# Optimization experiments

Hardware: AMD Instinct MI355X
Metric: run time of the kernel (lower is better)

Reference implementation:

```python
import jax, jax.numpy as jnp
import numpy as np

N = 8192
D = 512            # d_model
E = 8              # num_experts
H = 1024           # expert_hidden_dim
RH = 256           # router_hidden_dim
TOPK = 2
IN_DIM = 9 * D + 3
LN_EPS = 1e-5


def layernorm(x, g, b, eps=LN_EPS):
    m = jnp.mean(x, axis=-1, keepdims=True)
    v = jnp.mean((x - m) ** 2, axis=-1, keepdims=True)
    return (x - m) * jax.lax.rsqrt(v + eps) * g + b


def setup_inputs() -> dict:
    key = jax.random.key(0)
    ks = jax.random.split(key, 16)
    s_in = 1.0 / np.sqrt(IN_DIM)
    s_rh = 1.0 / np.sqrt(RH)
    s_h = 1.0 / np.sqrt(H)
    return {
        "z1": jax.random.normal(ks[0], (N, D), jnp.float32),
        "z2": jax.random.normal(ks[1], (N, D), jnp.float32),
        "z3": jax.random.normal(ks[2], (N, D), jnp.float32),
        "mask": jnp.ones((N, 3), jnp.float32),
        # LayerNorms
        "ln_g": jnp.ones((D,), jnp.float32), "ln_b": jnp.zeros((D,), jnp.float32),
        "lnp_g": jnp.ones((D,), jnp.float32), "lnp_b": jnp.zeros((D,), jnp.float32),
        "oln_g": jnp.ones((D,), jnp.float32), "oln_b": jnp.zeros((D,), jnp.float32),
        # Router MLP
        "r_w1": jax.random.normal(ks[3], (IN_DIM, RH), jnp.float32) * s_in,
        "r_b1": jnp.zeros((RH,), jnp.float32),
        "r_w2": jax.random.normal(ks[4], (RH, E), jnp.float32) * s_rh,
        "r_b2": jnp.zeros((E,), jnp.float32),
        "log_temp": jnp.array(np.log(1.0), jnp.float32),
        # Stacked experts: fc1 [E, IN_DIM, H], fc2 [E, H, D]
        "e_w1": jax.random.normal(ks[5], (E, IN_DIM, H), jnp.float32) * s_in,
        "e_b1": jnp.zeros((E, H), jnp.float32),
        "e_w2": jax.random.normal(ks[6], (E, H, D), jnp.float32) * s_h,
        "e_b2": jnp.zeros((E, D), jnp.float32),
    }


def reference(z1, z2, z3, mask, ln_g, ln_b, lnp_g, lnp_b, oln_g, oln_b,
              r_w1, r_b1, r_w2, r_b2, log_temp, e_w1, e_b1, e_w2, e_b2):
    # --- build fusion input ---
    z1n = layernorm(z1, ln_g, ln_b)
    z2n = layernorm(z2, ln_g, ln_b)
    z3n = layernorm(z3, ln_g, ln_b)
    d12 = layernorm(z1n - z2n, lnp_g, lnp_b)
    d13 = layernorm(z1n - z3n, lnp_g, lnp_b)
    d23 = layernorm(z2n - z3n, lnp_g, lnp_b)
    p12 = layernorm(z1n * z2n, lnp_g, lnp_b)
    p13 = layernorm(z1n * z3n, lnp_g, lnp_b)
    p23 = layernorm(z2n * z3n, lnp_g, lnp_b)
    x = jnp.concatenate([z1n, z2n, z3n, d12, d13, d23, p12, p13, p23, mask], axis=-1)  # [N, 9D+3]

    # --- router: MLP + temperature-scaled top-k softmax ---
    temp = jnp.clip(jnp.exp(log_temp), 1e-3, 100.0)
    rh = jax.nn.gelu(x @ r_w1 + r_b1, approximate=False)
    logits = (rh @ r_w2 + r_b2) / temp                      # [N, E]
    topv, topi = jax.lax.top_k(logits, TOPK)
    keep = jnp.zeros_like(logits).at[jnp.arange(logits.shape[0])[:, None], topi].set(1.0)
    masked_logits = jnp.where(keep == 0, -jnp.inf, logits)
    gate = jax.nn.softmax(masked_logits, axis=-1)           # [N, E]

    # --- dense expert compute (matches torch.stack over experts) ---
    eh = jax.nn.gelu(jnp.einsum('ni,eih->neh', x, e_w1) + e_b1, approximate=False)
    outs = jnp.einsum('neh,ehd->ned', eh, e_w2) + e_b2      # [N, E, D]
    z = jnp.einsum('ne,ned->nd', gate, outs)                # combine

    # --- masked residual ---
    denom = jnp.clip(jnp.sum(mask, axis=1, keepdims=True), 1.0, None)
    z_res = (mask[:, 0:1] * z1n + mask[:, 1:2] * z2n + mask[:, 2:3] * z3n) / denom
    z = z + z_res

    return layernorm(z, oln_g, oln_b)
```

## Files before the change

### kernel.cpp

```cpp
#include <hip/hip_runtime.h>
#include <math.h>

#define N_TOK 8192
#define DMODEL 512
#define NEXP 8
#define HEXP 1024
#define RHDIM 256
#define KP 4672
#define IN_REAL 4611
#define BK 64
#define NPAIR (N_TOK * 2)
#define MAXT 136
#define NRPART 8

typedef unsigned short u16;
typedef __bf16 bf16x8 __attribute__((ext_vector_type(8)));
typedef float f32x4 __attribute__((ext_vector_type(4)));

__device__ inline u16 f2bf(float f) {
    union { float f; unsigned u; } x; x.f = f;
    unsigned r = x.u + 0x7FFFu + ((x.u >> 16) & 1u);
    return (u16)(r >> 16);
}
__device__ inline float bf2f(u16 u) {
    union { unsigned u; float f; } x; x.u = ((unsigned)u) << 16;
    return x.f;
}
__device__ inline float gelu_exact(float v) {
    return 0.5f * v * (1.f + erff(v * 0.70710678118654752440f));
}

__device__ inline void async_cp16(const u16* g, u16* l) {
    __builtin_amdgcn_global_load_lds(
        (const __attribute__((address_space(1))) unsigned int*)g,
        (__attribute__((address_space(3))) unsigned int*)l, 16, 0, 0);
}

template<int M>
__device__ inline void bred128(float (&v)[M], int t, float* red) {
    #pragma unroll
    for (int o = 32; o > 0; o >>= 1)
        #pragma unroll
        for (int i = 0; i < M; i++) v[i] += __shfl_xor(v[i], o);
    __syncthreads();
    if ((t & 63) == 0) {
        #pragma unroll
        for (int i = 0; i < M; i++) red[(t >> 6) * M + i] = v[i];
    }
    __syncthreads();
    #pragma unroll
    for (int i = 0; i < M; i++) v[i] = red[i] + red[M + i];
}

__global__ __launch_bounds__(256)
void transpose_f32_bf16(const float* __restrict__ src, u16* __restrict__ dhi, u16* __restrict__ dlo,
                        int K0, int KPd, int H, size_t sbatch, size_t dbatch) {
    __shared__ float tile[32][33];
    int bz = blockIdx.z;
    src += (size_t)bz * sbatch;
    size_t dob = (size_t)bz * dbatch;
    int k0 = blockIdx.x * 32, h0 = blockIdx.y * 32;
    int tx = threadIdx.x, ty = threadIdx.y;
    for (int i = ty; i < 32; i += 8) {
        int k = k0 + i;
        tile[i][tx] = (k < K0) ? src[(size_t)k * H + (h0 + tx)] : 0.f;
    }
    __syncthreads();
    int tid = ty * 32 + tx;
    int h = tid >> 3, kq = tid & 7;
    int hg = h0 + h, kg = k0 + kq * 4;
    ushort4 hv, lv;
    float v0 = tile[kq * 4 + 0][h], v1 = tile[kq * 4 + 1][h];
    float v2 = tile[kq * 4 + 2][h], v3 = tile[kq * 4 + 3][h];
    hv.x = f2bf(v0); hv.y = f2bf(v1); hv.z = f2bf(v2); hv.w = f2bf(v3);
    *(ushort4*)(dhi + dob + (size_t)hg * KPd + kg) = hv;
    if (dlo) {
        lv.x = f2bf(v0 - bf2f(hv.x)); lv.y = f2bf(v1 - bf2f(hv.y));
        lv.z = f2bf(v2 - bf2f(hv.z)); lv.w = f2bf(v3 - bf2f(hv.w));
        *(ushort4*)(dlo + dob + (size_t)hg * KPd + kg) = lv;
    }
}

__global__ __launch_bounds__(128)
void build_x(const float* __restrict__ z1, const float* __restrict__ z2, const float* __restrict__ z3,
             const float* __restrict__ mask,
             const float* __restrict__ ln_g, const float* __restrict__ ln_b,
             const float* __restrict__ lnp_g, const float* __restrict__ lnp_b,
             u16* __restrict__ xhi, u16* __restrict__ xlo) {
    __shared__ float red[24];
    int n = blockIdx.x, t = threadIdx.x;
    int d0 = t * 4;
    float4 a4 = ((const float4*)(z1 + (size_t)n * DMODEL))[t];
    float4 b4 = ((const float4*)(z2 + (size_t)n * DMODEL))[t];
    float4 c4 = ((const float4*)(z3 + (size_t)n * DMODEL))[t];
    float a[4] = {a4.x, a4.y, a4.z, a4.w};
    float b[4] = {b4.x, b4.y, b4.z, b4.w};
    float c[4] = {c4.x, c4.y, c4.z, c4.w};
    float4 gg4 = ((const float4*)ln_g)[t], bb4 = ((const float4*)ln_b)[t];
    float4 pg4 = ((const float4*)lnp_g)[t], pb4 = ((const float4*)lnp_b)[t];
    float gg[4] = {gg4.x, gg4.y, gg4.z, gg4.w}, bb[4] = {bb4.x, bb4.y, bb4.z, bb4.w};
    float pg[4] = {pg4.x, pg4.y, pg4.z, pg4.w}, pb[4] = {pb4.x, pb4.y, pb4.z, pb4.w};
    size_t base = (size_t)n * KP;

    auto emit = [&](int seg, const float* v) {
        ushort4 hv, lv;
        hv.x = f2bf(v[0]); hv.y = f2bf(v[1]); hv.z = f2bf(v[2]); hv.w = f2bf(v[3]);
        lv.x = f2bf(v[0] - bf2f(hv.x)); lv.y = f2bf(v[1] - bf2f(hv.y));
        lv.z = f2bf(v[2] - bf2f(hv.z)); lv.w = f2bf(v[3] - bf2f(hv.w));
        *(ushort4*)(xhi + base + seg * DMODEL + d0) = hv;
        *(ushort4*)(xlo + base + seg * DMODEL + d0) = lv;
    };
    float v6[6] = {0.f, 0.f, 0.f, 0.f, 0.f, 0.f};
    #pragma unroll
    for (int j = 0; j < 4; j++) {
        v6[0] += a[j]; v6[1] += a[j] * a[j];
        v6[2] += b[j]; v6[3] += b[j] * b[j];
        v6[4] += c[j]; v6[5] += c[j] * c[j];
    }
    bred128<6>(v6, t, red);
    auto lnstats = [](float s, float q, float* m, float* r) {
        *m = s * (1.f / 512.f);
        float var = fmaxf(q * (1.f / 512.f) - (*m) * (*m), 0.f);
        *r = rsqrtf(var + 1e-5f);
    };
    float m1, r1, m2, r2, m3, r3;
    lnstats(v6[0], v6[1], &m1, &r1);
    lnstats(v6[2], v6[3], &m2, &r2);
    lnstats(v6[4], v6[5], &m3, &r3);
    float za[4], zb[4], zc[4];
    #pragma unroll
    for (int j = 0; j < 4; j++) {
        za[j] = (a[j] - m1) * r1 * gg[j] + bb[j];
        zb[j] = (b[j] - m2) * r2 * gg[j] + bb[j];
        zc[j] = (c[j] - m3) * r3 * gg[j] + bb[j];
    }
    emit(0, za); emit(1, zb); emit(2, zc);
    float d12[4], d13[4], d23[4], p12[4], p13[4], p23[4];
    float v12[12];
    #pragma unroll
    for (int i = 0; i < 12; i++) v12[i] = 0.f;
    #pragma unroll
    for (int j = 0; j < 4; j++) {
        d12[j] = za[j] - zb[j]; d13[j] = za[j] - zc[j]; d23[j] = zb[j] - zc[j];
        p12[j] = za[j] * zb[j]; p13[j] = za[j] * zc[j]; p23[j] = zb[j] * zc[j];
        v12[0] += d12[j]; v12[1] += d12[j] * d12[j];
        v12[2] += d13[j]; v12[3] += d13[j] * d13[j];
        v12[4] += d23[j]; v12[5] += d23[j] * d23[j];
        v12[6] += p12[j]; v12[7] += p12[j] * p12[j];
        v12[8] += p13[j]; v12[9] += p13[j] * p13[j];
        v12[10] += p23[j]; v12[11] += p23[j] * p23[j];
    }
    bred128<12>(v12, t, red);
    float* segs[6] = {d12, d13, d23, p12, p13, p23};
    #pragma unroll
    for (int s = 0; s < 6; s++) {
        float ms, rs;
        lnstats(v12[s * 2], v12[s * 2 + 1], &ms, &rs);
        float v[4];
        #pragma unroll
        for (int j = 0; j < 4; j++) v[j] = (segs[s][j] - ms) * rs * pg[j] + pb[j];
        emit(3 + s, v);
    }
    if (t < 16) {
        float v[4] = {0.f, 0.f, 0.f, 0.f};
        if (t == 0) { v[0] = mask[(size_t)n * 3]; v[1] = mask[(size_t)n * 3 + 1]; v[2] = mask[(size_t)n * 3 + 2]; }
        ushort4 hv, lv;
        hv.x = f2bf(v[0]); hv.y = f2bf(v[1]); hv.z = f2bf(v[2]); hv.w = f2bf(v[3]);
        lv.x = f2bf(v[0] - bf2f(hv.x)); lv.y = f2bf(v[1] - bf2f(hv.y));
        lv.z = f2bf(v[2] - bf2f(hv.z)); lv.w = f2bf(v[3] - bf2f(hv.w));
        *(ushort4*)(xhi + base + 9 * DMODEL + t * 4) = hv;
        *(ushort4*)(xlo + base + 9 * DMODEL + t * 4) = lv;
    }
}

#define GEMM_DEFS4                                                            \
    int t = threadIdx.x;                                                      \
    int lane = t & 63, w = t >> 6;                                            \
    int r8 = lane >> 3;                                                       \
    int ce = ((lane & 7) ^ r8) * 8;         \
    int fr = lane & 15, q4 = lane >> 4;                                       \
    int wm = (w & 1) * 64, wn = (w >> 1) * 64;                                \
    f32x4 acc[4][4];                                                          \
    { f32x4 z4 = {0.f, 0.f, 0.f, 0.f};                                        \
      _Pragma("unroll") for (int i = 0; i < 4; i++)                           \
      _Pragma("unroll") for (int j = 0; j < 4; j++) acc[i][j] = z4; }         \
    u16 *lAp[4], *lBp[4];                                                     \
    _Pragma("unroll") for (int i = 0; i < 4; i++) {                           \
        lAp[i] = lA + (w * 32 + 8 * i) * BK;                                  \
        lBp[i] = lB + (w * 32 + 8 * i) * BK;                                  \
    }

#define GEMM_KSTEP4                                                           \
        __syncthreads();                                                      \
        _Pragma("unroll") for (int i = 0; i < 4; i++) {                       \
            async_cp16(gA[i], lAp[i]); async_cp16(gB[i], lBp[i]);             \
            gA[i] += BK; gB[i] += BK;                                         \
        }                                                                     \
        __syncthreads();                                                      \
        _Pragma("unroll") for (int ks = 0; ks < 2; ks++) {                    \
            bf16x8 af[4], bfr[4];                                             \
            int cofs = (((q4 + ks * 4) ^ (fr & 7)) * 8);                      \
            _Pragma("unroll") for (int i = 0; i < 4; i++)                     \
                af[i] = *(const bf16x8*)&lA[(wm + i * 16 + fr) * BK + cofs];  \
            _Pragma("unroll") for (int j = 0; j < 4; j++)                     \
                bfr[j] = *(const bf16x8*)&lB[(wn + j * 16 + fr) * BK + cofs]; \
            _Pragma("unroll") for (int i = 0; i < 4; i++)                     \
            _Pragma("unroll") for (int j = 0; j < 4; j++)                     \
                acc[i][j] = __builtin_amdgcn_mfma_f32_16x16x32_bf16(af[i], bfr[j], acc[i][j], 0, 0, 0); \
        }

#define GEMM_DEFS8                                                            \
    int t = threadIdx.x;                                                      \
    int lane = t & 63, w = t >> 6;                                            \
    int r8 = lane >> 3;                                                       \
    int ce = ((lane & 7) ^ r8) * 8;         \
    int fr = lane & 15, q4 = lane >> 4;                                       \
    int wm = (w & 1) * 64, wn = (w >> 1) * 64;                                \
    f32x4 acc[4][4];                                                          \
    { f32x4 z4 = {0.f, 0.f, 0.f, 0.f};                                        \
      _Pragma("unroll") for (int i = 0; i < 4; i++)                           \
      _Pragma("unroll") for (int j = 0; j < 4; j++) acc[i][j] = z4; }         \
    u16 *lAp[2], *lBp[4];                                                     \
    _Pragma("unroll") for (int i = 0; i < 2; i++)                             \
        lAp[i] = lA + (w * 16 + 8 * i) * BK;                                  \
    _Pragma("unroll") for (int i = 0; i < 4; i++)                             \
        lBp[i] = lB + (w * 32 + 8 * i) * BK;

#define GEMM_KSTEP8                                                           \
        __syncthreads();                                                      \
        _Pragma("unroll") for (int i = 0; i < 2; i++) {                       \
            async_cp16(gA[i], lAp[i]); gA[i] += BK;                           \
        }                                                                     \
        _Pragma("unroll") for (int i = 0; i < 4; i++) {                       \
            async_cp16(gB[i], lBp[i]); gB[i] += BK;                           \
        }                                                                     \
        __syncthreads();                                                      \
        _Pragma("unroll") for (int ks = 0; ks < 2; ks++) {                    \
            bf16x8 af[4], bfr[4];                                             \
            int cofs = (((q4 + ks * 4) ^ (fr & 7)) * 8);                      \
            _Pragma("unroll") for (int i = 0; i < 4; i++)                     \
                af[i] = *(const bf16x8*)&lA[(wm + i * 16 + fr) * BK + cofs];  \
            _Pragma("unroll") for (int j = 0; j < 4; j++)                     \
                bfr[j] = *(const bf16x8*)&lB[(wn + j * 16 + fr) * BK + cofs]; \
            _Pragma("unroll") for (int i = 0; i < 4; i++)                     \
            _Pragma("unroll") for (int j = 0; j < 4; j++)                     \
                acc[i][j] = __builtin_amdgcn_mfma_f32_16x16x32_bf16(af[i], bfr[j], acc[i][j], 0, 0, 0); \
        }

__global__ __launch_bounds__(512, 4)
void router_fc1(const u16* __restrict__ xhi, const u16* __restrict__ xlo,
                const u16* __restrict__ rw1hi, const u16* __restrict__ rw1lo,
                float* __restrict__ rpart) {
    int mt = blockIdx.x & 63, part = blockIdx.x >> 6;
    const u16* A; const u16* B;
    int kbase, klen;
    if (part < 4) {
        A = xhi; B = rw1hi;
        kbase = part * 1152;
        klen = (part == 3) ? 1216 : 1152;
    } else {
        int half = part & 1;
        kbase = half ? 2304 : 0;
        klen  = half ? 2368 : 2304;
        if (part < 6) { A = xhi; B = rw1lo; }
        else          { A = xlo; B = rw1hi; }
    }

    __shared__ u16 lA[128 * BK];
    __shared__ u16 lB[256 * BK];
    GEMM_DEFS8

    const u16* gA[2]; const u16* gB[4];
    #pragma unroll
    for (int i = 0; i < 2; i++)
        gA[i] = A + (size_t)(mt * 128 + w * 16 + 8 * i + r8) * KP + kbase + ce;
    #pragma unroll
    for (int i = 0; i < 4; i++)
        gB[i] = B + (size_t)(w * 32 + 8 * i + r8) * KP + kbase + ce;

    for (int k0 = 0; k0 < klen; k0 += BK) {
        GEMM_KSTEP8
    }
    float* outp = rpart + (size_t)part * ((size_t)N_TOK * RHDIM);
    int cn = lane & 15;
    #pragma unroll
    for (int i = 0; i < 4; i++)
        #pragma unroll
        for (int rr = 0; rr < 4; rr++) {
            int mg = mt * 128 + wm + i * 16 + q4 * 4 + rr;
            #pragma unroll
            for (int j = 0; j < 4; j++)
                outp[(size_t)mg * RHDIM + wn + j * 16 + cn] = acc[i][j][rr];
        }
}

__global__ __launch_bounds__(256)
void logits_topk(const float* __restrict__ rpart, const float* __restrict__ r_b1,
                 const float* __restrict__ r_w2, const float* __restrict__ r_b2,
                 const float* __restrict__ log_temp,
                 float* __restrict__ pgate, int* __restrict__ pexp,
                 int* __restrict__ lists, int* __restrict__ counts) {
    int t = threadIdx.x, wave = t >> 6, lane = t & 63;
    int n = blockIdx.x * 4 + wave;
    float4 v = {0.f, 0.f, 0.f, 0.f};
    #pragma unroll
    for (int p = 0; p < NRPART; p++) {
        float4 s = ((const float4*)(rpart + (size_t)p * ((size_t)N_TOK * RHDIM) + (size_t)n * RHDIM))[lane];
        v.x += s.x; v.y += s.y; v.z += s.z; v.w += s.w;
    }
    float4 b1 = ((const float4*)r_b1)[lane];
    float rh0 = gelu_exact(v.x + b1.x);
    float rh1 = gelu_exact(v.y + b1.y);
    float rh2 = gelu_exact(v.z + b1.z);
    float rh3 = gelu_exact(v.w + b1.w);
    int k = lane * 4;
    float p8[8];
    #pragma unroll
    for (int e = 0; e < 8; e++)
        p8[e] = rh0 * r_w2[(k + 0) * 8 + e] + rh1 * r_w2[(k + 1) * 8 + e]
              + rh2 * r_w2[(k + 2) * 8 + e] + rh3 * r_w2[(k + 3) * 8 + e];
    #pragma unroll
    for (int o = 32; o > 0; o >>= 1)
        #pragma unroll
        for (int e = 0; e < 8; e++) p8[e] += __shfl_xor(p8[e], o);
    if (lane == 0) {
        float temp = fminf(fmaxf(expf(log_temp[0]), 1e-3f), 100.f);
        float l[8];
        #pragma unroll
        for (int e = 0; e < 8; e++) l[e] = (p8[e] + r_b2[e]) / temp;
        int i1 = 0;
        #pragma unroll
        for (int i = 1; i < 8; i++) if (l[i] > l[i1]) i1 = i;
        int i2 = (i1 == 0) ? 1 : 0;
        #pragma unroll
        for (int i = 0; i < 8; i++) if (i != i1 && l[i] > l[i2]) i2 = i;
        float p = expf(l[i2] - l[i1]);
        float g1 = 1.f / (1.f + p);
        float g2 = p / (1.f + p);
        pgate[n * 2] = g1;     pexp[n * 2] = i1;
        pgate[n * 2 + 1] = g2; pexp[n * 2 + 1] = i2;
        int pos1 = atomicAdd(&counts[i1], 1);
        lists[(size_t)i1 * N_TOK + pos1] = n * 2;
        int pos2 = atomicAdd(&counts[i2], 1);
        lists[(size_t)i2 * N_TOK + pos2] = n * 2 + 1;
    }
}

__global__ void sched_tiles(const int* __restrict__ counts, int* __restrict__ tiles) {
    if (threadIdx.x == 0) {
        int tcount = 0;
        for (int e = 0; e < NEXP; e++) {
            int nt = (counts[e] + 127) >> 7;
            for (int mt = 0; mt < nt; mt++) tiles[tcount++] = (e << 16) | mt;
        }
        for (; tcount < MAXT; tcount++) tiles[tcount] = -1;
    }
}

__global__ __launch_bounds__(256, 4)
void expert_fc1(const u16* __restrict__ xhi, const u16* __restrict__ w1t,
                const float* __restrict__ e_b1, const int* __restrict__ lists,
                const int* __restrict__ counts, const int* __restrict__ tiles,
                u16* __restrict__ eh) {
    int nt = blockIdx.x & 7, ti = blockIdx.x >> 3;
    int info = tiles[ti];
    if (info < 0) return;
    int e = info >> 16, mt = info & 0xFFFF;
    int cnt = counts[e];

    __shared__ u16 lA[128 * BK];
    __shared__ u16 lB[128 * BK];
    __shared__ int rows[128];
    int tt = threadIdx.x;
    if (tt < 128) {
        int m = mt * 128 + tt;
        rows[tt] = lists[(size_t)e * N_TOK + (m < cnt ? m : 0)];
    }
    __syncthreads();

    GEMM_DEFS4

    const u16* wb = w1t + (size_t)e * HEXP * KP + (size_t)(nt * 128) * KP;
    const u16* gA[4]; const u16* gB[4];
    #pragma unroll
    for (int i = 0; i < 4; i++) {
        gA[i] = xhi + (size_t)(rows[w * 32 + 8 * i + r8] >> 1) * KP + ce;
        gB[i] = wb + (size_t)(w * 32 + 8 * i + r8) * KP + ce;
    }

    for (int k0 = 0; k0 < KP; k0 += BK) {
        GEMM_KSTEP4
    }
    int cn = lane & 15;
    #pragma unroll
    for (int i = 0; i < 4; i++)
        #pragma unroll
        for (int rr = 0; rr < 4; rr++) {
            int ml = wm + i * 16 + q4 * 4 + rr;
            int mg = mt * 128 + ml;
            if (mg < cnt) {
                int entry = rows[ml];
                #pragma unroll
                for (int j = 0; j < 4; j++) {
                    int col = nt * 128 + wn + j * 16 + cn;
                    float v = acc[i][j][rr] + e_b1[(size_t)e * HEXP + col];
                    eh[(size_t)entry * HEXP + col] = f2bf(gelu_exact(v));
                }
            }
        }
}

__global__ __launch_bounds__(512, 4)
void expert_fc2(const u16* __restrict__ eh, const u16* __restrict__ w2t,
                const int* __restrict__ lists, const int* __restrict__ counts,
                const int* __restrict__ tiles, float* __restrict__ outs) {
    int nt = blockIdx.x & 1, ti = blockIdx.x >> 1;
    int info = tiles[ti];
    if (info < 0) return;
    int e = info >> 16, mt = info & 0xFFFF;
    int cnt = counts[e];

    __shared__ u16 lA[128 * BK];
    __shared__ u16 lB[256 * BK];
    __shared__ int rows[128];
    int tt = threadIdx.x;
    if (tt < 128) {
        int m = mt * 128 + tt;
        rows[tt] = lists[(size_t)e * N_TOK + (m < cnt ? m : 0)];
    }
    __syncthreads();

    GEMM_DEFS8

    const u16* wb = w2t + (size_t)e * DMODEL * HEXP + (size_t)(nt * 256) * HEXP;
    const u16* gA[2]; const u16* gB[4];
    #pragma unroll
    for (int i = 0; i < 2; i++)
        gA[i] = eh + (size_t)rows[w * 16 + 8 * i + r8] * HEXP + ce;
    #pragma unroll
    for (int i = 0; i < 4; i++)
        gB[i] = wb + (size_t)(w * 32 + 8 * i + r8) * HEXP + ce;

    for (int k0 = 0; k0 < HEXP; k0 += BK) {
        GEMM_KSTEP8
    }
    int cn = lane & 15;
    #pragma unroll
    for (int i = 0; i < 4; i++)
        #pragma unroll
        for (int rr = 0; rr < 4; rr++) {
            int ml = wm + i * 16 + q4 * 4 + rr;
            int mg = mt * 128 + ml;
            if (mg < cnt) {
                int entry = rows[ml];
                #pragma unroll
                for (int j = 0; j < 4; j++) {
                    int col = nt * 256 + wn + j * 16 + cn;
                    outs[(size_t)entry * DMODEL + col] = acc[i][j][rr];
                }
            }
        }
}

__global__ __launch_bounds__(128)
void combine_ln(const float* __restrict__ outs, const float* __restrict__ pgate,
                const int* __restrict__ pexp, const float* __restrict__ e_b2,
                const float* __restrict__ mask, const u16* __restrict__ xhi,
                const u16* __restrict__ xlo, const float* __restrict__ oln_g,
                const float* __restrict__ oln_b, float* __restrict__ out) {
    __shared__ float red[4];
    int n = blockIdx.x, t = threadIdx.x;
    float g0 = pgate[n * 2], g1 = pgate[n * 2 + 1];
    int e0 = pexp[n * 2], e1 = pexp[n * 2 + 1];
    float4 o0 = ((const float4*)(outs + (size_t)(n * 2) * DMODEL))[t];
    float4 o1 = ((const float4*)(outs + (size_t)(n * 2 + 1) * DMODEL))[t];
    float4 b0 = ((const float4*)(e_b2 + (size_t)e0 * DMODEL))[t];
    float4 b1 = ((const float4*)(e_b2 + (size_t)e1 * DMODEL))[t];
    float o[4] = {g0 * (o0.x + b0.x) + g1 * (o1.x + b1.x),
                  g0 * (o0.y + b0.y) + g1 * (o1.y + b1.y),
                  g0 * (o0.z + b0.z) + g1 * (o1.z + b1.z),
                  g0 * (o0.w + b0.w) + g1 * (o1.w + b1.w)};
    float m0 = mask[n * 3 + 0], m1 = mask[n * 3 + 1], m2 = mask[n * 3 + 2];
    float denom = fmaxf(m0 + m1 + m2, 1.f);
    size_t xb = (size_t)n * KP;
    ushort4 h1 = *(const ushort4*)(xhi + xb + t * 4);
    ushort4 l1 = *(const ushort4*)(xlo + xb + t * 4);
    ushort4 h2 = *(const ushort4*)(xhi + xb + DMODEL + t * 4);
    ushort4 l2 = *(const ushort4*)(xlo + xb + DMODEL + t * 4);
    ushort4 h3 = *(const ushort4*)(xhi + xb + 2 * DMODEL + t * 4);
    ushort4 l3 = *(const ushort4*)(xlo + xb + 2 * DMODEL + t * 4);
    float z[4], s = 0.f, q = 0.f;
    u16 h1a[4] = {h1.x, h1.y, h1.z, h1.w}, l1a[4] = {l1.x, l1.y, l1.z, l1.w};
    u16 h2a[4] = {h2.x, h2.y, h2.z, h2.w}, l2a[4] = {l2.x, l2.y, l2.z, l2.w};
    u16 h3a[4] = {h3.x, h3.y, h3.z, h3.w}, l3a[4] = {l3.x, l3.y, l3.z, l3.w};
    #pragma unroll
    for (int j = 0; j < 4; j++) {
        float z1n = bf2f(h1a[j]) + bf2f(l1a[j]);
        float z2n = bf2f(h2a[j]) + bf2f(l2a[j]);
        float z3n = bf2f(h3a[j]) + bf2f(l3a[j]);
        z[j] = o[j] + (m0 * z1n + m1 * z2n + m2 * z3n) / denom;
        s += z[j]; q += z[j] * z[j];
    }
    #pragma unroll
    for (int ofs = 32; ofs > 0; ofs >>= 1) {
        s += __shfl_xor(s, ofs);
        q += __shfl_xor(q, ofs);
    }
    if ((t & 63) == 0) { red[(t >> 6) * 2] = s; red[(t >> 6) * 2 + 1] = q; }
    __syncthreads();
    s = red[0] + red[2]; q = red[1] + red[3];
    float m = s * (1.f / 512.f);
    float var = fmaxf(q * (1.f / 512.f) - m * m, 0.f);
    float r = rsqrtf(var + 1e-5f);
    float4 g4 = ((const float4*)oln_g)[t], be4 = ((const float4*)oln_b)[t];
    float4 res;
    res.x = (z[0] - m) * r * g4.x + be4.x;
    res.y = (z[1] - m) * r * g4.y + be4.y;
    res.z = (z[2] - m) * r * g4.z + be4.z;
    res.w = (z[3] - m) * r * g4.w + be4.w;
    ((float4*)(out + (size_t)n * DMODEL))[t] = res;
}

extern "C" void kernel_launch(void* const* d_in, const int* in_sizes, int n_in,
                              void* d_out, int out_size, void* d_ws, size_t ws_size,
                              hipStream_t stream) {
    (void)in_sizes; (void)n_in; (void)out_size; (void)ws_size;
    const float* z1       = (const float*)d_in[0];
    const float* z2       = (const float*)d_in[1];
    const float* z3       = (const float*)d_in[2];
    const float* mask     = (const float*)d_in[3];
    const float* ln_g     = (const float*)d_in[4];
    const float* ln_b     = (const float*)d_in[5];
    const float* lnp_g    = (const float*)d_in[6];
    const float* lnp_b    = (const float*)d_in[7];
    const float* oln_g    = (const float*)d_in[8];
    const float* oln_b    = (const float*)d_in[9];
    const float* r_w1     = (const float*)d_in[10];
    const float* r_b1     = (const float*)d_in[11];
    const float* r_w2     = (const float*)d_in[12];
    const float* r_b2     = (const float*)d_in[13];
    const float* log_temp = (const float*)d_in[14];
    const float* e_w1     = (const float*)d_in[15];
    const float* e_b1     = (const float*)d_in[16];
    const float* e_w2     = (const float*)d_in[17];
    const float* e_b2     = (const float*)d_in[18];
    float* out = (float*)d_out;

    char* p = (char*)d_ws;
    auto carve = [&](size_t bytes) { char* r = p; p += (bytes + 255) & ~(size_t)255; return r; };
    u16*   xhi    = (u16*)carve((size_t)N_TOK * KP * 2);
    u16*   xlo    = (u16*)carve((size_t)N_TOK * KP * 2);
    u16*   w1t    = (u16*)carve((size_t)NEXP * HEXP * KP * 2);
    u16*   w2t    = (u16*)carve((size_t)NEXP * DMODEL * HEXP * 2);
    u16*   rw1hi  = (u16*)carve((size_t)RHDIM * KP * 2);
    u16*   rw1lo  = (u16*)carve((size_t)RHDIM * KP * 2);
    float* rpart  = (float*)carve((size_t)NRPART * N_TOK * RHDIM * 4);
    u16*   eh     = (u16*)carve((size_t)NPAIR * HEXP * 2);
    float* outsb  = (float*)carve((size_t)NPAIR * DMODEL * 4);
    float* pgate  = (float*)carve((size_t)NPAIR * 4);
    int*   pexp   = (int*)carve((size_t)NPAIR * 4);
    int*   lists  = (int*)carve((size_t)NEXP * N_TOK * 4);
    int*   counts = (int*)carve(256);
    int*   tiles  = (int*)carve(MAXT * 4);

    dim3 tb(32, 8);
    transpose_f32_bf16<<<dim3(KP / 32, HEXP / 32, NEXP), tb, 0, stream>>>(
        e_w1, w1t, (u16*)nullptr, IN_REAL, KP, HEXP, (size_t)IN_REAL * HEXP, (size_t)HEXP * KP);
    transpose_f32_bf16<<<dim3(HEXP / 32, DMODEL / 32, NEXP), tb, 0, stream>>>(
        e_w2, w2t, (u16*)nullptr, HEXP, HEXP, DMODEL, (size_t)HEXP * DMODEL, (size_t)DMODEL * HEXP);
    transpose_f32_bf16<<<dim3(KP / 32, RHDIM / 32, 1), tb, 0, stream>>>(
        r_w1, rw1hi, rw1lo, IN_REAL, KP, RHDIM, (size_t)0, (size_t)0);

    build_x<<<N_TOK, 128, 0, stream>>>(z1, z2, z3, mask, ln_g, ln_b, lnp_g, lnp_b, xhi, xlo);

    router_fc1<<<512, 512, 0, stream>>>(xhi, xlo, rw1hi, rw1lo, rpart);

    hipMemsetAsync(counts, 0, 256, stream);
    logits_topk<<<N_TOK / 4, 256, 0, stream>>>(rpart, r_b1, r_w2, r_b2, log_temp,
                                               pgate, pexp, lists, counts);
    sched_tiles<<<1, 64, 0, stream>>>(counts, tiles);

    expert_fc1<<<MAXT * 8, 256, 0, stream>>>(xhi, w1t, e_b1, lists, counts, tiles, eh);
    expert_fc2<<<MAXT * 2, 512, 0, stream>>>(eh, w2t, lists, counts, tiles, outsb);

    combine_ln<<<N_TOK, 128, 0, stream>>>(outsb, pgate, pexp, e_b2, mask, xhi, xlo, oln_g, oln_b, out);
}
```

Measured before the change: 923.5 us.

## Fuse prep kernels into one launch and drop tile scheduler kernel

Merges the three weight-transpose kernels and build_x into a single prep_all launch that dispatches on block index, with build_x now processing two tokens per 256-thread block. Removes the single-thread sched_tiles kernel. Expert fc1/fc2 now launch a fixed worst-case grid indexed by expert and tile, and blocks beyond the expert's count exit early. The aim is fewer launches and dependent serial steps, at the cost of many empty blocks launched and an expert-interleaved block order.

Result: slower. 1.055 ms (+14.2%).

```diff
diff --git a/kernel.cpp b/kernel.cpp
--- a/kernel.cpp
+++ b/kernel.cpp
@@ -10,8 +10,13 @@
 #define IN_REAL 4611
 #define BK 64
 #define NPAIR (N_TOK * 2)
-#define MAXT 136
 #define NRPART 8
+
+#define TR1_BLOCKS (146 * 32 * 8)
+#define TR2_BLOCKS (32 * 16 * 8)
+#define TR3_BLOCKS (146 * 8)
+#define BX_BLOCKS  (N_TOK / 2)
+#define PREP_BLOCKS (TR1_BLOCKS + TR2_BLOCKS + TR3_BLOCKS + BX_BLOCKS)
 
 typedef unsigned short u16;
 typedef __bf16 bf16x8 __attribute__((ext_vector_type(8)));
@@ -37,67 +42,94 @@
 }
 
 template<int M>
-__device__ inline void bred128(float (&v)[M], int t, float* red) {
+__device__ inline void bred128(float (&v)[M], int tl, float* red) {
     #pragma unroll
     for (int o = 32; o > 0; o >>= 1)
         #pragma unroll
         for (int i = 0; i < M; i++) v[i] += __shfl_xor(v[i], o);
     __syncthreads();
-    if ((t & 63) == 0) {
-        #pragma unroll
-        for (int i = 0; i < M; i++) red[(t >> 6) * M + i] = v[i];
+    if ((tl & 63) == 0) {
+        #pragma unroll
+        for (int i = 0; i < M; i++) red[(tl >> 6) * M + i] = v[i];
     }
     __syncthreads();
     #pragma unroll
     for (int i = 0; i < M; i++) v[i] = red[i] + red[M + i];
 }
 
-__global__ __launch_bounds__(256)
-void transpose_f32_bf16(const float* __restrict__ src, u16* __restrict__ dhi, u16* __restrict__ dlo,
-                        int K0, int KPd, int H, size_t sbatch, size_t dbatch) {
-    __shared__ float tile[32][33];
-    int bz = blockIdx.z;
-    src += (size_t)bz * sbatch;
-    size_t dob = (size_t)bz * dbatch;
-    int k0 = blockIdx.x * 32, h0 = blockIdx.y * 32;
-    int tx = threadIdx.x, ty = threadIdx.y;
+__device__ inline void tr_tile(const float* __restrict__ src, u16* __restrict__ dhi,
+                               u16* __restrict__ dlo, int K0, int KPd, int H,
+                               int k0, int h0, size_t dob, float (*tile)[33]) {
+    int t = threadIdx.x;
+    int tx = t & 31, ty = t >> 5;
     for (int i = ty; i < 32; i += 8) {
         int k = k0 + i;
         tile[i][tx] = (k < K0) ? src[(size_t)k * H + (h0 + tx)] : 0.f;
     }
     __syncthreads();
-    int tid = ty * 32 + tx;
-    int h = tid >> 3, kq = tid & 7;
+    int h = t >> 3, kq = t & 7;
     int hg = h0 + h, kg = k0 + kq * 4;
-    ushort4 hv, lv;
     float v0 = tile[kq * 4 + 0][h], v1 = tile[kq * 4 + 1][h];
     float v2 = tile[kq * 4 + 2][h], v3 = tile[kq * 4 + 3][h];
+    ushort4 hv;
     hv.x = f2bf(v0); hv.y = f2bf(v1); hv.z = f2bf(v2); hv.w = f2bf(v3);
     *(ushort4*)(dhi + dob + (size_t)hg * KPd + kg) = hv;
     if (dlo) {
+        ushort4 lv;
         lv.x = f2bf(v0 - bf2f(hv.x)); lv.y = f2bf(v1 - bf2f(hv.y));
         lv.z = f2bf(v2 - bf2f(hv.z)); lv.w = f2bf(v3 - bf2f(hv.w));
         *(ushort4*)(dlo + dob + (size_t)hg * KPd + kg) = lv;
     }
 }
 
-__global__ __launch_bounds__(128)
-void build_x(const float* __restrict__ z1, const float* __restrict__ z2, const float* __restrict__ z3,
-             const float* __restrict__ mask,
-             const float* __restrict__ ln_g, const float* __restrict__ ln_b,
-             const float* __restrict__ lnp_g, const float* __restrict__ lnp_b,
-             u16* __restrict__ xhi, u16* __restrict__ xlo) {
-    __shared__ float red[24];
-    int n = blockIdx.x, t = threadIdx.x;
-    int d0 = t * 4;
-    float4 a4 = ((const float4*)(z1 + (size_t)n * DMODEL))[t];
-    float4 b4 = ((const float4*)(z2 + (size_t)n * DMODEL))[t];
-    float4 c4 = ((const float4*)(z3 + (size_t)n * DMODEL))[t];
+__global__ __launch_bounds__(256)
+void prep_all(const float* __restrict__ e_w1, const float* __restrict__ e_w2,
+              const float* __restrict__ r_w1,
+              u16* __restrict__ w1t, u16* __restrict__ w2t,
+              u16* __restrict__ rw1hi, u16* __restrict__ rw1lo,
+              const float* __restrict__ z1, const float* __restrict__ z2,
+              const float* __restrict__ z3, const float* __restrict__ mask,
+              const float* __restrict__ ln_g, const float* __restrict__ ln_b,
+              const float* __restrict__ lnp_g, const float* __restrict__ lnp_b,
+              u16* __restrict__ xhi, u16* __restrict__ xlo) {
+    __shared__ float tile[32][33];
+    __shared__ float red[48];
+    int b = blockIdx.x;
+    if (b < TR1_BLOCKS) {
+        int e = b / 4672, r = b % 4672;
+        tr_tile(e_w1 + (size_t)e * IN_REAL * HEXP, w1t, (u16*)nullptr,
+                IN_REAL, KP, HEXP, (r % 146) * 32, (r / 146) * 32,
+                (size_t)e * HEXP * KP, tile);
+        return;
+    }
+    b -= TR1_BLOCKS;
+    if (b < TR2_BLOCKS) {
+        int e = b / 512, r = b % 512;
+        tr_tile(e_w2 + (size_t)e * HEXP * DMODEL, w2t, (u16*)nullptr,
+                HEXP, HEXP, DMODEL, (r % 32) * 32, (r / 32) * 32,
+                (size_t)e * DMODEL * HEXP, tile);
+        return;
+    }
+    b -= TR2_BLOCKS;
+    if (b < TR3_BLOCKS) {
+        tr_tile(r_w1, rw1hi, rw1lo, IN_REAL, KP, RHDIM,
+                (b % 146) * 32, (b / 146) * 32, (size_t)0, tile);
+        return;
+    }
+    b -= TR3_BLOCKS;
+    int t = threadIdx.x;
+    int tl = t & 127;
+    int n = b * 2 + (t >> 7);
+    float* redh = red + (t >> 7) * 24;
+    int d0 = tl * 4;
+    float4 a4 = ((const float4*)(z1 + (size_t)n * DMODEL))[tl];
+    float4 b4 = ((const float4*)(z2 + (size_t)n * DMODEL))[tl];
+    float4 c4 = ((const float4*)(z3 + (size_t)n * DMODEL))[tl];
     float a[4] = {a4.x, a4.y, a4.z, a4.w};
-    float b[4] = {b4.x, b4.y, b4.z, b4.w};
+    float bb_[4] = {b4.x, b4.y, b4.z, b4.w};
     float c[4] = {c4.x, c4.y, c4.z, c4.w};
-    float4 gg4 = ((const float4*)ln_g)[t], bb4 = ((const float4*)ln_b)[t];
-    float4 pg4 = ((const float4*)lnp_g)[t], pb4 = ((const float4*)lnp_b)[t];
+    float4 gg4 = ((const float4*)ln_g)[tl], bb4 = ((const float4*)ln_b)[tl];
+    float4 pg4 = ((const float4*)lnp_g)[tl], pb4 = ((const float4*)lnp_b)[tl];
     float gg[4] = {gg4.x, gg4.y, gg4.z, gg4.w}, bb[4] = {bb4.x, bb4.y, bb4.z, bb4.w};
     float pg[4] = {pg4.x, pg4.y, pg4.z, pg4.w}, pb[4] = {pb4.x, pb4.y, pb4.z, pb4.w};
     size_t base = (size_t)n * KP;
@@ -110,19 +142,19 @@
         *(ushort4*)(xhi + base + seg * DMODEL + d0) = hv;
         *(ushort4*)(xlo + base + seg * DMODEL + d0) = lv;
     };
-    float v6[6] = {0.f, 0.f, 0.f, 0.f, 0.f, 0.f};
-    #pragma unroll
-    for (int j = 0; j < 4; j++) {
-        v6[0] += a[j]; v6[1] += a[j] * a[j];
-        v6[2] += b[j]; v6[3] += b[j] * b[j];
-        v6[4] += c[j]; v6[5] += c[j] * c[j];
-    }
-    bred128<6>(v6, t, red);
     auto lnstats = [](float s, float q, float* m, float* r) {
         *m = s * (1.f / 512.f);
         float var = fmaxf(q * (1.f / 512.f) - (*m) * (*m), 0.f);
         *r = rsqrtf(var + 1e-5f);
     };
+    float v6[6] = {0.f, 0.f, 0.f, 0.f, 0.f, 0.f};
+    #pragma unroll
+    for (int j = 0; j < 4; j++) {
+        v6[0] += a[j]; v6[1] += a[j] * a[j];
+        v6[2] += bb_[j]; v6[3] += bb_[j] * bb_[j];
+        v6[4] += c[j]; v6[5] += c[j] * c[j];
+    }
+    bred128<6>(v6, tl, redh);
     float m1, r1, m2, r2, m3, r3;
     lnstats(v6[0], v6[1], &m1, &r1);
     lnstats(v6[2], v6[3], &m2, &r2);
@@ -131,7 +163,7 @@
     #pragma unroll
     for (int j = 0; j < 4; j++) {
         za[j] = (a[j] - m1) * r1 * gg[j] + bb[j];
-        zb[j] = (b[j] - m2) * r2 * gg[j] + bb[j];
+        zb[j] = (bb_[j] - m2) * r2 * gg[j] + bb[j];
         zc[j] = (c[j] - m3) * r3 * gg[j] + bb[j];
     }
     emit(0, za); emit(1, zb); emit(2, zc);
@@ -150,7 +182,7 @@
         v12[8] += p13[j]; v12[9] += p13[j] * p13[j];
         v12[10] += p23[j]; v12[11] += p23[j] * p23[j];
     }
-    bred128<12>(v12, t, red);
+    bred128<12>(v12, tl, redh);
     float* segs[6] = {d12, d13, d23, p12, p13, p23};
     #pragma unroll
     for (int s = 0; s < 6; s++) {
@@ -161,15 +193,15 @@
         for (int j = 0; j < 4; j++) v[j] = (segs[s][j] - ms) * rs * pg[j] + pb[j];
         emit(3 + s, v);
     }
-    if (t < 16) {
+    if (tl < 16) {
         float v[4] = {0.f, 0.f, 0.f, 0.f};
-        if (t == 0) { v[0] = mask[(size_t)n * 3]; v[1] = mask[(size_t)n * 3 + 1]; v[2] = mask[(size_t)n * 3 + 2]; }
+        if (tl == 0) { v[0] = mask[(size_t)n * 3]; v[1] = mask[(size_t)n * 3 + 1]; v[2] = mask[(size_t)n * 3 + 2]; }
         ushort4 hv, lv;
         hv.x = f2bf(v[0]); hv.y = f2bf(v[1]); hv.z = f2bf(v[2]); hv.w = f2bf(v[3]);
         lv.x = f2bf(v[0] - bf2f(hv.x)); lv.y = f2bf(v[1] - bf2f(hv.y));
         lv.z = f2bf(v[2] - bf2f(hv.z)); lv.w = f2bf(v[3] - bf2f(hv.w));
-        *(ushort4*)(xhi + base + 9 * DMODEL + t * 4) = hv;
-        *(ushort4*)(xlo + base + 9 * DMODEL + t * 4) = lv;
+        *(ushort4*)(xhi + base + 9 * DMODEL + tl * 4) = hv;
+        *(ushort4*)(xlo + base + 9 * DMODEL + tl * 4) = lv;
     }
 }
 
@@ -346,27 +378,15 @@
     }
 }
 
-__global__ void sched_tiles(const int* __restrict__ counts, int* __restrict__ tiles) {
-    if (threadIdx.x == 0) {
-        int tcount = 0;
-        for (int e = 0; e < NEXP; e++) {
-            int nt = (counts[e] + 127) >> 7;
-            for (int mt = 0; mt < nt; mt++) tiles[tcount++] = (e << 16) | mt;
-        }
-        for (; tcount < MAXT; tcount++) tiles[tcount] = -1;
-    }
-}
-
 __global__ __launch_bounds__(256, 4)
 void expert_fc1(const u16* __restrict__ xhi, const u16* __restrict__ w1t,
                 const float* __restrict__ e_b1, const int* __restrict__ lists,
-                const int* __restrict__ counts, const int* __restrict__ tiles,
-                u16* __restrict__ eh) {
-    int nt = blockIdx.x & 7, ti = blockIdx.x >> 3;
-    int info = tiles[ti];
-    if (info < 0) return;
-    int e = info >> 16, mt = info & 0xFFFF;
+                const int* __restrict__ counts, u16* __restrict__ eh) {
+    int e = blockIdx.x & 7;
+    int k = blockIdx.x >> 3;
+    int mt = k >> 3, nt = k & 7;
     int cnt = counts[e];
+    if (mt * 128 >= cnt) return;
 
     __shared__ u16 lA[128 * BK];
     __shared__ u16 lB[128 * BK];
@@ -413,12 +433,12 @@
 __global__ __launch_bounds__(512, 4)
 void expert_fc2(const u16* __restrict__ eh, const u16* __restrict__ w2t,
                 const int* __restrict__ lists, const int* __restrict__ counts,
-                const int* __restrict__ tiles, float* __restrict__ outs) {
-    int nt = blockIdx.x & 1, ti = blockIdx.x >> 1;
-    int info = tiles[ti];
-    if (info < 0) return;
-    int e = info >> 16, mt = info & 0xFFFF;
+                float* __restrict__ outs) {
+    int e = blockIdx.x & 7;
+    int k = blockIdx.x >> 3;
+    int mt = k >> 1, nt = k & 1;
     int cnt = counts[e];
+    if (mt * 128 >= cnt) return;
 
     __shared__ u16 lA[128 * BK];
     __shared__ u16 lB[256 * BK];
@@ -561,27 +581,19 @@
     int*   pexp   = (int*)carve((size_t)NPAIR * 4);
     int*   lists  = (int*)carve((size_t)NEXP * N_TOK * 4);
     int*   counts = (int*)carve(256);
-    int*   tiles  = (int*)carve(MAXT * 4);
-
-    dim3 tb(32, 8);
-    transpose_f32_bf16<<<dim3(KP / 32, HEXP / 32, NEXP), tb, 0, stream>>>(
-        e_w1, w1t, (u16*)nullptr, IN_REAL, KP, HEXP, (size_t)IN_REAL * HEXP, (size_t)HEXP * KP);
-    transpose_f32_bf16<<<dim3(HEXP / 32, DMODEL / 32, NEXP), tb, 0, stream>>>(
-        e_w2, w2t, (u16*)nullptr, HEXP, HEXP, DMODEL, (size_t)HEXP * DMODEL, (size_t)DMODEL * HEXP);
-    transpose_f32_bf16<<<dim3(KP / 32, RHDIM / 32, 1), tb, 0, stream>>>(
-        r_w1, rw1hi, rw1lo, IN_REAL, KP, RHDIM, (size_t)0, (size_t)0);
-
-    build_x<<<N_TOK, 128, 0, stream>>>(z1, z2, z3, mask, ln_g, ln_b, lnp_g, lnp_b, xhi, xlo);
+
+    prep_all<<<PREP_BLOCKS, 256, 0, stream>>>(
+        e_w1, e_w2, r_w1, w1t, w2t, rw1hi, rw1lo,
+        z1, z2, z3, mask, ln_g, ln_b, lnp_g, lnp_b, xhi, xlo);
 
     router_fc1<<<512, 512, 0, stream>>>(xhi, xlo, rw1hi, rw1lo, rpart);
 
     hipMemsetAsync(counts, 0, 256, stream);
     logits_topk<<<N_TOK / 4, 256, 0, stream>>>(rpart, r_b1, r_w2, r_b2, log_temp,
                                                pgate, pexp, lists, counts);
-    sched_tiles<<<1, 64, 0, stream>>>(counts, tiles);
-
-    expert_fc1<<<MAXT * 8, 256, 0, stream>>>(xhi, w1t, e_b1, lists, counts, tiles, eh);
-    expert_fc2<<<MAXT * 2, 512, 0, stream>>>(eh, w2t, lists, counts, tiles, outsb);
+
+    expert_fc1<<<8 * 128 * 8, 256, 0, stream>>>(xhi, w1t, e_b1, lists, counts, eh);
+    expert_fc2<<<8 * 128 * 2, 512, 0, stream>>>(eh, w2t, lists, counts, outsb);
 
     combine_ln<<<N_TOK, 128, 0, stream>>>(outsb, pgate, pexp, e_b2, mask, xhi, xlo, oln_g, oln_b, out);
 }
```
